# Performance work log

Measured on AMD Instinct MI355X. Metric: run time of the kernel, lower is better.

Reference implementation:

```python
import jax, jax.numpy as jnp
import numpy as np

N_LAYERS, D_MODEL, D_INNER, D_STATE, DT_RANK, D_CONV, VOCAB = 4, 768, 1536, 16, 48, 4, 32000
B, L = 2, 512
EPS = 1e-5


def rmsnorm(x, w):
    var = jnp.mean(jnp.square(x), axis=-1, keepdims=True)
    return x * jax.lax.rsqrt(var + EPS) * w


def mamba_mixer(x, in_w, cw, cb, xp_w, dtp_w, dtp_b, A_log, D_sk, out_w):
    # x: [B, L, D]
    proj = x @ in_w.T                                   # [B, L, 2*d_inner]
    h, gate = jnp.split(proj, 2, axis=-1)
    hc = jnp.transpose(h, (0, 2, 1))                    # [B, d_inner, L]
    hc = jax.lax.conv_general_dilated(
        hc, cw[:, None, :], (1,), [(D_CONV - 1, 0)],
        dimension_numbers=('NCH', 'OIH', 'NCH'),
        feature_group_count=D_INNER) + cb[None, :, None]  # causal depthwise conv
    h = jax.nn.silu(jnp.transpose(hc, (0, 2, 1)))       # [B, L, d_inner]
    ssm = h @ xp_w.T                                    # [B, L, dt_rank + 2*d_state]
    dt, Bm, Cm = jnp.split(ssm, [DT_RANK, DT_RANK + D_STATE], axis=-1)
    dt = jax.nn.softplus(dt @ dtp_w.T + dtp_b)          # [B, L, d_inner]
    A = -jnp.exp(A_log)                                 # [d_inner, d_state], always negative
    dA = jnp.exp(dt[..., None] * A)                     # [B, L, d_inner, d_state]
    dBu = (dt * h)[..., None] * Bm[:, :, None, :]       # [B, L, d_inner, d_state]

    def step(state, inp):
        dA_t, dBu_t, C_t = inp
        state = dA_t * state + dBu_t                    # [B, d_inner, d_state]
        return state, jnp.einsum('bds,bs->bd', state, C_t)

    xs = (jnp.moveaxis(dA, 1, 0), jnp.moveaxis(dBu, 1, 0), jnp.moveaxis(Cm, 1, 0))
    init = jnp.zeros((x.shape[0], D_INNER, D_STATE), dtype=x.dtype)
    _, ys = jax.lax.scan(step, init, xs)                # ys: [L, B, d_inner]
    y = jnp.moveaxis(ys, 0, 1) + D_sk * h
    y = y * jax.nn.silu(gate)
    return y @ out_w.T                                  # [B, L, D]


def setup_inputs() -> dict:
    key = jax.random.key(0)
    ks = jax.random.split(key, 8)
    inp = {
        'input_ids': jax.random.randint(ks[0], (B, L), 0, VOCAB, dtype=jnp.int32),
        'embed': jax.random.normal(ks[1], (VOCAB, D_MODEL), jnp.float32) * 0.02,
        'norm_f_w': jnp.ones((D_MODEL,), jnp.float32),
        'in_proj_w': jax.random.normal(ks[2], (N_LAYERS, 2 * D_INNER, D_MODEL), jnp.float32) * (D_MODEL ** -0.5),
        'conv_w': jax.random.normal(ks[3], (N_LAYERS, D_INNER, D_CONV), jnp.float32) * 0.3,
        'conv_b': jnp.zeros((N_LAYERS, D_INNER), jnp.float32),
        'x_proj_w': jax.random.normal(ks[4], (N_LAYERS, DT_RANK + 2 * D_STATE, D_INNER), jnp.float32) * (D_INNER ** -0.5),
        'dt_proj_w': jax.random.normal(ks[5], (N_LAYERS, D_INNER, DT_RANK), jnp.float32) * (DT_RANK ** -0.5),
        'dt_proj_b': jax.random.normal(ks[6], (N_LAYERS, D_INNER), jnp.float32) * 0.1,
        'A_log': jnp.broadcast_to(jnp.log(jnp.arange(1, D_STATE + 1, dtype=jnp.float32)), (N_LAYERS, D_INNER, D_STATE)).copy(),
        'D_skip': jnp.ones((N_LAYERS, D_INNER), jnp.float32),
        'out_proj_w': jax.random.normal(ks[7], (N_LAYERS, D_MODEL, D_INNER), jnp.float32) * (D_INNER ** -0.5),
        'norm_w': jnp.ones((N_LAYERS, D_MODEL), jnp.float32),
    }
    return inp


def reference(input_ids, embed, norm_f_w, in_proj_w, conv_w, conv_b,
              x_proj_w, dt_proj_w, dt_proj_b, A_log, D_skip, out_proj_w, norm_w):
    h = embed[input_ids]                                # [B, L, D]
    for i in range(N_LAYERS):
        h = h + mamba_mixer(rmsnorm(h, norm_w[i]), in_proj_w[i], conv_w[i], conv_b[i],
                            x_proj_w[i], dt_proj_w[i], dt_proj_b[i],
                            A_log[i], D_skip[i], out_proj_w[i])
    h = rmsnorm(h, norm_f_w)
    return h @ embed.T                                  # tied lm head logits [B, L, VOCAB]
```

## Files before the change

### kernel.cpp

```cpp
#include <hip/hip_runtime.h>
#include <hip/hip_bf16.h>
#include <math.h>

#define NL 4
#define DM 768
#define DI 1536
#define DS 16
#define DTR 48
#define DCONV 4
#define VOCAB_ 32000
#define BB 2
#define LL 512
#define ROWS (BB*LL)
#define SSMW (DTR + 2*DS)
#define NC 32
#define CL (LL/NC)
#define NDB (DI/16)
#define XP_KS 16
#define XP_KC (DI/XP_KS)
#define OP_KS 4
#define OP_KC (DI/OP_KS)

typedef __bf16 bf16x8 __attribute__((ext_vector_type(8)));
typedef float f32x4 __attribute__((ext_vector_type(4)));

__device__ __forceinline__ unsigned short f2bf(float f) {
    unsigned u = __float_as_uint(f);
    u = u + 0x7fffu + ((u >> 16) & 1u);
    return (unsigned short)(u >> 16);
}
__device__ __forceinline__ float bf2f(unsigned short b) {
    return __uint_as_float((unsigned)b << 16);
}

__global__ __launch_bounds__(256) void split_kernel(
    const float* __restrict__ x,
    unsigned short* __restrict__ hi, unsigned short* __restrict__ lo, int n4)
{
    int i = blockIdx.x * 256 + threadIdx.x;
    if (i >= n4) return;
    const float4 v = ((const float4*)x)[i];
    float vv[4] = {v.x, v.y, v.z, v.w};
    unsigned short hh[4], ll[4];
    #pragma unroll
    for (int j = 0; j < 4; j++) {
        hh[j] = f2bf(vv[j]);
        ll[j] = f2bf(vv[j] - bf2f(hh[j]));
    }
    ((ushort4*)hi)[i] = make_ushort4(hh[0], hh[1], hh[2], hh[3]);
    ((ushort4*)lo)[i] = make_ushort4(ll[0], ll[1], ll[2], ll[3]);
}

__device__ __forceinline__ void gld16(void* l, const void* g) {
    __builtin_amdgcn_global_load_lds(
        (const __attribute__((address_space(1))) void*)g,
        (__attribute__((address_space(3))) void*)l, 16, 0, 0);
}

template<int EPI>
__global__ __launch_bounds__(256) void gemm_mfma(
    const unsigned short* __restrict__ Ahi, const unsigned short* __restrict__ Alo, int lda,
    const unsigned short* __restrict__ Bhi, const unsigned short* __restrict__ Blo, int ldb,
    float* __restrict__ C, int ldc, int K,
    const float* __restrict__ resid, int gx, size_t zstride)
{
    __shared__ __align__(16) unsigned short sAh[128*32];
    __shared__ __align__(16) unsigned short sAl[128*32];
    __shared__ __align__(16) unsigned short sBh[128*32];
    __shared__ __align__(16) unsigned short sBl[128*32];

    const int tid  = threadIdx.x;
    const int lane = tid & 63;
    const int nb = gridDim.x;
    const int v  = (blockIdx.x & 7) * (nb >> 3) + (blockIdx.x >> 3);
    const int m0 = (v % gx) * 128;
    const int n0 = (v / gx) * 128;
    const int kb = (int)blockIdx.y * K;
    C += (size_t)blockIdx.y * zstride;

    const int w  = tid >> 6;
    const int wr = (w >> 1) * 64;
    const int wc = (w & 1) * 64;

    f32x4 acc[4][4];
    #pragma unroll
    for (int i = 0; i < 4; i++)
        #pragma unroll
        for (int j = 0; j < 4; j++)
            acc[i][j] = (f32x4){0.f, 0.f, 0.f, 0.f};

    const int srow = tid >> 2;
    const int ps   = tid & 3;
    const int lsl  = ps ^ ((srow >> 1) & 3);

    int offA[4], offB[4];
    #pragma unroll
    for (int i = 0; i < 4; i++) {
        int ra = wr + i*16 + (lane & 15);
        int pa = (lane >> 4) ^ ((ra >> 1) & 3);
        offA[i] = ra*32 + pa*8;
        int rb = wc + i*16 + (lane & 15);
        int pb = (lane >> 4) ^ ((rb >> 1) & 3);
        offB[i] = rb*32 + pb*8;
    }

    for (int k0 = kb; k0 < kb + K; k0 += 32) {
        const size_t a1 = (size_t)(m0 + srow)      * lda + k0 + lsl*8;
        const size_t a2 = (size_t)(m0 + 64 + srow) * lda + k0 + lsl*8;
        const size_t b1 = (size_t)(n0 + srow)      * ldb + k0 + lsl*8;
        const size_t b2 = (size_t)(n0 + 64 + srow) * ldb + k0 + lsl*8;
        gld16(&sAh[(size_t)tid*8],       Ahi + a1);
        gld16(&sAh[(size_t)(256+tid)*8], Ahi + a2);
        gld16(&sAl[(size_t)tid*8],       Alo + a1);
        gld16(&sAl[(size_t)(256+tid)*8], Alo + a2);
        gld16(&sBh[(size_t)tid*8],       Bhi + b1);
        gld16(&sBh[(size_t)(256+tid)*8], Bhi + b2);
        gld16(&sBl[(size_t)tid*8],       Blo + b1);
        gld16(&sBl[(size_t)(256+tid)*8], Blo + b2);
        __syncthreads();

        bf16x8 ah[4], al[4], bh[4], bl[4];
        #pragma unroll
        for (int i = 0; i < 4; i++) {
            ah[i] = *(const bf16x8*)&sAh[offA[i]];
            al[i] = *(const bf16x8*)&sAl[offA[i]];
            bh[i] = *(const bf16x8*)&sBh[offB[i]];
            bl[i] = *(const bf16x8*)&sBl[offB[i]];
        }
        #pragma unroll
        for (int i = 0; i < 4; i++)
            #pragma unroll
            for (int j = 0; j < 4; j++) {
                acc[i][j] = __builtin_amdgcn_mfma_f32_16x16x32_bf16(ah[i], bh[j], acc[i][j], 0, 0, 0);
                acc[i][j] = __builtin_amdgcn_mfma_f32_16x16x32_bf16(ah[i], bl[j], acc[i][j], 0, 0, 0);
                acc[i][j] = __builtin_amdgcn_mfma_f32_16x16x32_bf16(al[i], bh[j], acc[i][j], 0, 0, 0);
            }
        __syncthreads();
    }

    #pragma unroll
    for (int i = 0; i < 4; i++) {
        int rbase = m0 + wr + i*16 + (lane >> 4)*4;
        #pragma unroll
        for (int j = 0; j < 4; j++) {
            int col = n0 + wc + j*16 + (lane & 15);
            #pragma unroll
            for (int r = 0; r < 4; r++) {
                float vv = acc[i][j][r];
                if (EPI == 2) vv += resid[(size_t)(rbase + r)*ldc + col];
                C[(size_t)(rbase + r)*ldc + col] = vv;
            }
        }
    }
}

__global__ __launch_bounds__(256) void opart_reduce_kernel(
    const float* __restrict__ part, float* __restrict__ h, int n)
{
    int i = blockIdx.x * 256 + threadIdx.x;
    if (i >= n) return;
    float s = h[i];
    #pragma unroll
    for (int z = 0; z < OP_KS; ++z)
        s += part[(size_t)z * n + i];
    h[i] = s;
}

__global__ __launch_bounds__(256) void gather_kernel(
    const int* __restrict__ ids, const float* __restrict__ embed,
    float* __restrict__ h, int n)
{
    int idx = blockIdx.x * 256 + threadIdx.x;
    if (idx >= n) return;
    int d = idx % DM;
    int tok = idx / DM;
    h[idx] = embed[(size_t)ids[tok] * DM + d];
}

__global__ __launch_bounds__(256) void rmsnorm_kernel(
    const float* __restrict__ x, const float* __restrict__ w,
    float* __restrict__ out, int D)
{
    int row = blockIdx.x;
    const float* xr = x + (size_t)row * D;
    float ss = 0.f;
    for (int i = threadIdx.x; i < D; i += 256) { float v = xr[i]; ss += v * v; }
    for (int o = 32; o >= 1; o >>= 1) ss += __shfl_xor(ss, o, 64);
    __shared__ float sbuf[4];
    int wid = threadIdx.x >> 6;
    if ((threadIdx.x & 63) == 0) sbuf[wid] = ss;
    __syncthreads();
    if (threadIdx.x == 0) {
        float t = sbuf[0] + sbuf[1] + sbuf[2] + sbuf[3];
        sbuf[0] = 1.0f / sqrtf(t / (float)D + 1e-5f);
    }
    __syncthreads();
    float scale = sbuf[0];
    for (int i = threadIdx.x; i < D; i += 256)
        out[(size_t)row * D + i] = xr[i] * scale * w[i];
}

__global__ __launch_bounds__(256) void rmsnorm_split_kernel(
    const float* __restrict__ x, const float* __restrict__ w,
    unsigned short* __restrict__ hi, unsigned short* __restrict__ lo, int D)
{
    int row = blockIdx.x;
    const float* xr = x + (size_t)row * D;
    float ss = 0.f;
    for (int i = threadIdx.x; i < D; i += 256) { float v = xr[i]; ss += v * v; }
    for (int o = 32; o >= 1; o >>= 1) ss += __shfl_xor(ss, o, 64);
    __shared__ float sbuf[4];
    int wid = threadIdx.x >> 6;
    if ((threadIdx.x & 63) == 0) sbuf[wid] = ss;
    __syncthreads();
    if (threadIdx.x == 0) {
        float t = sbuf[0] + sbuf[1] + sbuf[2] + sbuf[3];
        sbuf[0] = 1.0f / sqrtf(t / (float)D + 1e-5f);
    }
    __syncthreads();
    float scale = sbuf[0];
    for (int i = threadIdx.x; i < D; i += 256) {
        float v = xr[i] * scale * w[i];
        unsigned short hh = f2bf(v);
        hi[(size_t)row * D + i] = hh;
        lo[(size_t)row * D + i] = f2bf(v - bf2f(hh));
    }
}

template<int EPI>
__global__ __launch_bounds__(256) void gemm_tn(
    const float* __restrict__ A, int lda,
    const float* __restrict__ W, int ldw,
    float* __restrict__ C, int ldc,
    int M, int N, int K,
    const float* __restrict__ bias,
    const float* __restrict__ resid)
{
    const int tid = threadIdx.x;
    const int tx = tid & 15;
    const int ty = tid >> 4;
    const int m0 = blockIdx.x * 64;
    const int n0 = blockIdx.y * 64;

    __shared__ float As[16][65];
    __shared__ float Ws[16][65];

    float acc[4][4];
    #pragma unroll
    for (int i = 0; i < 4; i++)
        #pragma unroll
        for (int j = 0; j < 4; j++) acc[i][j] = 0.f;

    const int lrow = tid >> 2;
    const int lk   = (tid & 3) * 4;

    for (int k0 = 0; k0 < K; k0 += 16) {
        {
            int m = m0 + lrow;
            int n = n0 + lrow;
            #pragma unroll
            for (int j = 0; j < 4; j++) {
                int k = k0 + lk + j;
                As[lk + j][lrow] = (m < M && k < K) ? A[(size_t)m * lda + k] : 0.f;
                Ws[lk + j][lrow] = (n < N && k < K) ? W[(size_t)n * ldw + k] : 0.f;
            }
        }
        __syncthreads();
        #pragma unroll
        for (int k = 0; k < 16; k++) {
            float a[4], wv[4];
            #pragma unroll
            for (int i = 0; i < 4; i++) a[i] = As[k][ty * 4 + i];
            #pragma unroll
            for (int j = 0; j < 4; j++) wv[j] = Ws[k][tx * 4 + j];
            #pragma unroll
            for (int i = 0; i < 4; i++)
                #pragma unroll
                for (int j = 0; j < 4; j++)
                    acc[i][j] += a[i] * wv[j];
        }
        __syncthreads();
    }

    #pragma unroll
    for (int i = 0; i < 4; i++) {
        int m = m0 + ty * 4 + i;
        if (m >= M) continue;
        #pragma unroll
        for (int j = 0; j < 4; j++) {
            int n = n0 + tx * 4 + j;
            if (n >= N) continue;
            float v = acc[i][j];
            if (EPI == 1) {
                v += bias[n];
                v = fmaxf(v, 0.f) + log1pf(expf(-fabsf(v)));
            }
            if (EPI == 2) v += resid[(size_t)m * ldc + n];
            C[(size_t)m * ldc + n] = v;
        }
    }
}

__global__ __launch_bounds__(256) void xproj_partial_kernel(
    const float* __restrict__ A,
    const float* __restrict__ W,
    float* __restrict__ part)
{
    __shared__ float sA[32*97];
    __shared__ float sW[80*97];
    const int m0 = blockIdx.x * 32;
    const int k0 = blockIdx.y * XP_KC;

    for (int idx = threadIdx.x; idx < 32*XP_KC; idx += 256) {
        int r = idx / XP_KC, k = idx % XP_KC;
        sA[r*97 + k] = A[(size_t)(m0 + r)*DI + k0 + k];
    }
    for (int idx = threadIdx.x; idx < 80*XP_KC; idx += 256) {
        int r = idx / XP_KC, k = idx % XP_KC;
        sW[r*97 + k] = W[(size_t)r*DI + k0 + k];
    }
    __syncthreads();

    const int tr = (threadIdx.x >> 4) * 2;
    const int tc = (threadIdx.x & 15) * 5;
    float acc[2][5];
    #pragma unroll
    for (int i = 0; i < 2; i++)
        #pragma unroll
        for (int j = 0; j < 5; j++) acc[i][j] = 0.f;

    #pragma unroll 4
    for (int k = 0; k < XP_KC; ++k) {
        float a0 = sA[tr*97 + k];
        float a1 = sA[(tr+1)*97 + k];
        float w0 = sW[(tc+0)*97 + k];
        float w1 = sW[(tc+1)*97 + k];
        float w2 = sW[(tc+2)*97 + k];
        float w3 = sW[(tc+3)*97 + k];
        float w4 = sW[(tc+4)*97 + k];
        acc[0][0] += a0*w0; acc[0][1] += a0*w1; acc[0][2] += a0*w2;
        acc[0][3] += a0*w3; acc[0][4] += a0*w4;
        acc[1][0] += a1*w0; acc[1][1] += a1*w1; acc[1][2] += a1*w2;
        acc[1][3] += a1*w3; acc[1][4] += a1*w4;
    }

    float* pp = part + ((size_t)blockIdx.y * ROWS + m0) * SSMW;
    #pragma unroll
    for (int i = 0; i < 2; i++)
        #pragma unroll
        for (int j = 0; j < 5; j++)
            pp[(size_t)(tr + i)*SSMW + tc + j] = acc[i][j];
}

__global__ __launch_bounds__(256) void xproj_reduce_kernel(
    const float* __restrict__ part, float* __restrict__ ssmout)
{
    int i = blockIdx.x * 256 + threadIdx.x;
    if (i >= ROWS * SSMW) return;
    float s = 0.f;
    #pragma unroll
    for (int ks = 0; ks < XP_KS; ++ks)
        s += part[(size_t)ks * ROWS * SSMW + i];
    ssmout[i] = s;
}

__global__ __launch_bounds__(256) void conv_silu_kernel(
    const float* __restrict__ proj,
    const float* __restrict__ cw, const float* __restrict__ cb,
    float* __restrict__ hconv)
{
    int idx = blockIdx.x * 256 + threadIdx.x;
    if (idx >= ROWS * DI) return;
    int d = idx % DI;
    int bt = idx / DI;
    int t = bt % LL;
    float sum = cb[d];
    #pragma unroll
    for (int j = 0; j < DCONV; j++) {
        int tt = t - (DCONV - 1) + j;
        if (tt >= 0)
            sum += cw[d * DCONV + j] * proj[(size_t)(bt - (DCONV - 1) + j) * (2 * DI) + d];
    }
    float sig = 1.f / (1.f + expf(-sum));
    hconv[idx] = sum * sig;
}

__global__ __launch_bounds__(256) void scan_local_kernel(
    const float* __restrict__ dt, const float* __restrict__ hconv,
    const float* __restrict__ ssm, const float* __restrict__ A_log,
    float* __restrict__ ylocal, float* __restrict__ E, float* __restrict__ P)
{
    const int tid = threadIdx.x;
    const int s  = tid & 15;
    const int dg = tid >> 4;
    int blk = blockIdx.x;
    const int dblk = blk % NDB; blk /= NDB;
    const int c = blk % NC;
    const int b = blk / NC;
    const int d = dblk * 16 + dg;

    const float Ads = -expf(A_log[(size_t)d * DS + s]);
    float state = 0.f, Ssum = 0.f;
    const int t0 = c * CL;
    const float* dtp = dt     + ((size_t)b*LL + t0)*DI + d;
    const float* hp  = hconv  + ((size_t)b*LL + t0)*DI + d;
    const float* sp  = ssm    + ((size_t)b*LL + t0)*SSMW;
    float*       yp  = ylocal + ((size_t)b*LL + t0)*DI + d;

    for (int t = 0; t < CL; ++t) {
        float dtv = dtp[(size_t)t * DI];
        float hv  = hp[(size_t)t * DI];
        float Bv  = sp[(size_t)t * SSMW + DTR + s];
        float Cv  = sp[(size_t)t * SSMW + DTR + DS + s];
        float dA  = expf(dtv * Ads);
        state = dA * state + dtv * hv * Bv;
        Ssum += dtv;
        float contrib = state * Cv;
        contrib += __shfl_xor(contrib, 1, 16);
        contrib += __shfl_xor(contrib, 2, 16);
        contrib += __shfl_xor(contrib, 4, 16);
        contrib += __shfl_xor(contrib, 8, 16);
        if (s == 0) yp[(size_t)t * DI] = contrib;
    }
    const size_t si = (((size_t)b*NC + c)*DI + d)*DS + s;
    E[si] = state;
    P[si] = expf(Ads * Ssum);
}

__global__ __launch_bounds__(256) void scan_carry_kernel(
    const float* __restrict__ E, const float* __restrict__ P,
    float* __restrict__ carry)
{
    int g = blockIdx.x * 256 + threadIdx.x;
    if (g >= BB * DI * DS) return;
    int b   = g / (DI * DS);
    int dsi = g % (DI * DS);
    float cv = 0.f;
    for (int c = 0; c < NC; ++c) {
        size_t idx = ((size_t)b*NC + c)*(DI*DS) + dsi;
        carry[idx] = cv;
        cv = P[idx] * cv + E[idx];
    }
}

template<int PLANES>
__global__ __launch_bounds__(256) void scan_fix_kernel(
    const float* __restrict__ dt, const float* __restrict__ hconv,
    const float* __restrict__ ssm, const float* __restrict__ proj,
    const float* __restrict__ A_log, const float* __restrict__ D_skip,
    const float* __restrict__ carry, float* __restrict__ y,
    unsigned short* __restrict__ yhi, unsigned short* __restrict__ ylo)
{
    const int tid = threadIdx.x;
    const int s  = tid & 15;
    const int dg = tid >> 4;
    int blk = blockIdx.x;
    const int dblk = blk % NDB; blk /= NDB;
    const int c = blk % NC;
    const int b = blk / NC;
    const int d = dblk * 16 + dg;

    const float Ads = -expf(A_log[(size_t)d * DS + s]);
    const float Dd  = D_skip[d];
    const float cv  = carry[(((size_t)b*NC + c)*DI + d)*DS + s];
    float S = 0.f;
    const int t0 = c * CL;
    const float* dtp = dt    + ((size_t)b*LL + t0)*DI + d;
    const float* hp  = hconv + ((size_t)b*LL + t0)*DI + d;
    const float* sp  = ssm   + ((size_t)b*LL + t0)*SSMW;
    const float* gp  = proj  + ((size_t)b*LL + t0)*(2*DI) + DI + d;
    const size_t yoff = ((size_t)b*LL + t0)*DI + d;

    for (int t = 0; t < CL; ++t) {
        float dtv = dtp[(size_t)t * DI];
        S += dtv;
        float Cv = sp[(size_t)t * SSMW + DTR + DS + s];
        float contrib = expf(Ads * S) * cv * Cv;
        contrib += __shfl_xor(contrib, 1, 16);
        contrib += __shfl_xor(contrib, 2, 16);
        contrib += __shfl_xor(contrib, 4, 16);
        contrib += __shfl_xor(contrib, 8, 16);
        if (s == 0) {
            float hv  = hp[(size_t)t * DI];
            float ylv = y[yoff + (size_t)t * DI];
            float gv  = gp[(size_t)t * (2*DI)];
            float sig = 1.f / (1.f + expf(-gv));
            float yv  = (ylv + contrib + Dd * hv) * (gv * sig);
            if (PLANES) {
                unsigned short hh = f2bf(yv);
                yhi[yoff + (size_t)t * DI] = hh;
                ylo[yoff + (size_t)t * DI] = f2bf(yv - bf2f(hh));
            } else {
                y[yoff + (size_t)t * DI] = yv;
            }
        }
    }
}

extern "C" void kernel_launch(void* const* d_in, const int* in_sizes, int n_in,
                              void* d_out, int out_size, void* d_ws, size_t ws_size,
                              hipStream_t stream)
{
    const int*   ids        = (const int*)  d_in[0];
    const float* embed      = (const float*)d_in[1];
    const float* norm_f_w   = (const float*)d_in[2];
    const float* in_proj_w  = (const float*)d_in[3];
    const float* conv_w     = (const float*)d_in[4];
    const float* conv_b     = (const float*)d_in[5];
    const float* x_proj_w   = (const float*)d_in[6];
    const float* dt_proj_w  = (const float*)d_in[7];
    const float* dt_proj_b  = (const float*)d_in[8];
    const float* A_log      = (const float*)d_in[9];
    const float* D_skip     = (const float*)d_in[10];
    const float* out_proj_w = (const float*)d_in[11];
    const float* norm_w     = (const float*)d_in[12];
    float* out = (float*)d_out;

    float* ws    = (float*)d_ws;
    float* h     = ws;
    float* xn    = h     + ROWS * DM;
    float* proj  = xn    + ROWS * DM;
    float* hconv = proj  + ROWS * 2 * DI;
    float* ssm   = hconv + ROWS * DI;
    float* dtb   = ssm   + ROWS * SSMW;
    float* yb    = dtb   + ROWS * DI;
    float* Ebuf  = yb    + ROWS * DI;
    float* Pbuf  = Ebuf  + (size_t)BB*NC*DI*DS;
    float* cbuf  = Pbuf  + (size_t)BB*NC*DI*DS;
    float* xpart = cbuf  + (size_t)BB*NC*DI*DS;
    float* opart = xpart + (size_t)XP_KS*ROWS*SSMW;
    const size_t F32_FLOATS = (size_t)ROWS * (DM + DM + 2*DI + DI + SSMW + DI + DI)
                            + 3 * (size_t)BB*NC*DI*DS
                            + (size_t)XP_KS*ROWS*SSMW
                            + (size_t)OP_KS*ROWS*DM;

    const size_t IPW_E = (size_t)NL * 2 * DI * DM;
    const size_t OPW_E = (size_t)NL * DM * DI;
    const size_t ACT_E = (size_t)ROWS * DI;
    const size_t EMB_E = (size_t)VOCAB_ * DM;
    unsigned short* u0   = (unsigned short*)(ws + F32_FLOATS);
    unsigned short* ipwh = u0;
    unsigned short* ipwl = ipwh + IPW_E;
    unsigned short* opwh = ipwl + IPW_E;
    unsigned short* opwl = opwh + OPW_E;
    unsigned short* acth = opwl + OPW_E;
    unsigned short* actl = acth + ACT_E;
    unsigned short* embh = actl + ACT_E;
    unsigned short* embl = embh + EMB_E;
    const size_t NEED_PROJ = F32_FLOATS*4 + 2*2*(IPW_E + OPW_E + ACT_E);
    const size_t NEED_HEAD = NEED_PROJ + 2*2*EMB_E;
    const bool mfma_proj = ws_size >= NEED_PROJ;
    const bool mfma_head = ws_size >= NEED_HEAD;

    gather_kernel<<<(ROWS * DM + 255) / 256, 256, 0, stream>>>(ids, embed, h, ROWS * DM);

    if (mfma_proj) {
        split_kernel<<<(int)(IPW_E/4 + 255)/256, 256, 0, stream>>>(in_proj_w,  ipwh, ipwl, (int)(IPW_E/4));
        split_kernel<<<(int)(OPW_E/4 + 255)/256, 256, 0, stream>>>(out_proj_w, opwh, opwl, (int)(OPW_E/4));
    }
    if (mfma_head) {
        split_kernel<<<(int)(EMB_E/4 + 255)/256, 256, 0, stream>>>(embed, embh, embl, (int)(EMB_E/4));
    }

    for (int i = 0; i < NL; ++i) {
        const float* ipw = in_proj_w  + (size_t)i * 2 * DI * DM;
        const float* cw  = conv_w     + (size_t)i * DI * DCONV;
        const float* cb  = conv_b     + (size_t)i * DI;
        const float* xpw = x_proj_w   + (size_t)i * SSMW * DI;
        const float* dpw = dt_proj_w  + (size_t)i * DI * DTR;
        const float* dpb = dt_proj_b  + (size_t)i * DI;
        const float* al  = A_log      + (size_t)i * DI * DS;
        const float* dsk = D_skip     + (size_t)i * DI;
        const float* opw = out_proj_w + (size_t)i * DM * DI;
        const float* nw  = norm_w     + (size_t)i * DM;

        if (mfma_proj) {
            rmsnorm_split_kernel<<<ROWS, 256, 0, stream>>>(h, nw, acth, actl, DM);
            gemm_mfma<0><<<dim3(8*24, 1), 256, 0, stream>>>(
                acth, actl, DM, ipwh + (size_t)i*2*DI*DM, ipwl + (size_t)i*2*DI*DM, DM,
                proj, 2*DI, DM, nullptr, 8, 0);
        } else {
            rmsnorm_kernel<<<ROWS, 256, 0, stream>>>(h, nw, xn, DM);
            gemm_tn<0><<<dim3(ROWS/64, (2*DI)/64), 256, 0, stream>>>(
                xn, DM, ipw, DM, proj, 2*DI, ROWS, 2*DI, DM, nullptr, nullptr);
        }

        conv_silu_kernel<<<(ROWS * DI + 255) / 256, 256, 0, stream>>>(proj, cw, cb, hconv);

        xproj_partial_kernel<<<dim3(ROWS/32, XP_KS), 256, 0, stream>>>(hconv, xpw, xpart);
        xproj_reduce_kernel<<<(ROWS*SSMW + 255)/256, 256, 0, stream>>>(xpart, ssm);

        gemm_tn<1><<<dim3(ROWS / 64, DI / 64), 256, 0, stream>>>(
            ssm, SSMW, dpw, DTR, dtb, DI, ROWS, DI, DTR, dpb, nullptr);

        scan_local_kernel<<<BB*NC*NDB, 256, 0, stream>>>(dtb, hconv, ssm, al, yb, Ebuf, Pbuf);
        scan_carry_kernel<<<(BB*DI*DS + 255)/256, 256, 0, stream>>>(Ebuf, Pbuf, cbuf);

        if (mfma_proj) {
            scan_fix_kernel<1><<<BB*NC*NDB, 256, 0, stream>>>(
                dtb, hconv, ssm, proj, al, dsk, cbuf, yb, acth, actl);
            gemm_mfma<0><<<dim3(8*6, OP_KS), 256, 0, stream>>>(
                acth, actl, DI, opwh + (size_t)i*DM*DI, opwl + (size_t)i*DM*DI, DI,
                opart, DM, OP_KC, nullptr, 8, (size_t)ROWS*DM);
            opart_reduce_kernel<<<(ROWS*DM + 255)/256, 256, 0, stream>>>(opart, h, ROWS*DM);
        } else {
            scan_fix_kernel<0><<<BB*NC*NDB, 256, 0, stream>>>(
                dtb, hconv, ssm, proj, al, dsk, cbuf, yb, nullptr, nullptr);
            gemm_tn<2><<<dim3(ROWS/64, DM/64), 256, 0, stream>>>(
                yb, DI, opw, DI, h, DM, ROWS, DM, DI, nullptr, h);
        }
    }

    if (mfma_head) {
        rmsnorm_split_kernel<<<ROWS, 256, 0, stream>>>(h, norm_f_w, acth, actl, DM);
        gemm_mfma<0><<<dim3(8*250, 1), 256, 0, stream>>>(
            acth, actl, DM, embh, embl, DM, out, VOCAB_, DM, nullptr, 8, 0);
    } else {
        rmsnorm_kernel<<<ROWS, 256, 0, stream>>>(h, norm_f_w, xn, DM);
        gemm_tn<0><<<dim3(ROWS/64, VOCAB_/64), 256, 0, stream>>>(
            xn, DM, embed, DM, out, VOCAB_, ROWS, VOCAB_, DM, nullptr, nullptr);
    }
}
```

Before: 1.238 ms.

## Fuse reductions with norms, dt projection, and fold scan carry into fix kernel

Merges the embedding gather with the first RMSNorm+bf16 split, and the out-projection partial reduction with the next layer's (or final) RMSNorm+split. Fuses the x_proj split-K reduction with the dt projection GEMM and softplus. Removes the separate scan carry kernel by having each scan_fix block recompute its chunk carry serially from E/P. This cuts kernel launches and intermediate round trips, at the cost of redundant carry recomputation and x_proj reductions across blocks. If the workspace is too small for the MFMA path but large enough for the MFMA head, the head may read an uninitialised normalised buffer.

Measured after the change: 1.226 ms. Within noise of the previous version (-1.0%).

```diff
diff --git a/kernel.cpp b/kernel.cpp
--- a/kernel.cpp
+++ b/kernel.cpp
@@ -20,6 +20,7 @@
 #define XP_KC (DI/XP_KS)
 #define OP_KS 4
 #define OP_KC (DI/OP_KS)
+#define DTB 96
 
 typedef __bf16 bf16x8 __attribute__((ext_vector_type(8)));
 typedef float f32x4 __attribute__((ext_vector_type(4)));
@@ -154,18 +155,6 @@
     }
 }
 
-__global__ __launch_bounds__(256) void opart_reduce_kernel(
-    const float* __restrict__ part, float* __restrict__ h, int n)
-{
-    int i = blockIdx.x * 256 + threadIdx.x;
-    if (i >= n) return;
-    float s = h[i];
-    #pragma unroll
-    for (int z = 0; z < OP_KS; ++z)
-        s += part[(size_t)z * n + i];
-    h[i] = s;
-}
-
 __global__ __launch_bounds__(256) void gather_kernel(
     const int* __restrict__ ids, const float* __restrict__ embed,
     float* __restrict__ h, int n)
@@ -175,6 +164,77 @@
     int d = idx % DM;
     int tok = idx / DM;
     h[idx] = embed[(size_t)ids[tok] * DM + d];
+}
+
+__global__ __launch_bounds__(256) void gather_norm_kernel(
+    const int* __restrict__ ids, const float* __restrict__ embed,
+    const float* __restrict__ w, float* __restrict__ h,
+    unsigned short* __restrict__ hi, unsigned short* __restrict__ lo)
+{
+    __shared__ float buf[DM];
+    __shared__ float sbuf[4];
+    const int row = blockIdx.x;
+    const int tok = ids[row];
+    float ss = 0.f;
+    for (int i = threadIdx.x; i < DM; i += 256) {
+        float v = embed[(size_t)tok*DM + i];
+        h[(size_t)row*DM + i] = v;
+        buf[i] = v;
+        ss += v*v;
+    }
+    for (int o = 32; o >= 1; o >>= 1) ss += __shfl_xor(ss, o, 64);
+    int wid = threadIdx.x >> 6;
+    if ((threadIdx.x & 63) == 0) sbuf[wid] = ss;
+    __syncthreads();
+    if (threadIdx.x == 0) {
+        float t = sbuf[0]+sbuf[1]+sbuf[2]+sbuf[3];
+        sbuf[0] = 1.0f / sqrtf(t/(float)DM + 1e-5f);
+    }
+    __syncthreads();
+    float scale = sbuf[0];
+    for (int i = threadIdx.x; i < DM; i += 256) {
+        float v = buf[i]*scale*w[i];
+        unsigned short hh = f2bf(v);
+        hi[(size_t)row*DM+i] = hh;
+        lo[(size_t)row*DM+i] = f2bf(v - bf2f(hh));
+    }
+}
+
+__global__ __launch_bounds__(256) void opreduce_norm_kernel(
+    const float* __restrict__ part,
+    const float* __restrict__ w,
+    float* __restrict__ h,
+    unsigned short* __restrict__ hi, unsigned short* __restrict__ lo)
+{
+    __shared__ float buf[DM];
+    __shared__ float sbuf[4];
+    const int row = blockIdx.x;
+    float ss = 0.f;
+    for (int i = threadIdx.x; i < DM; i += 256) {
+        float v = h[(size_t)row*DM + i];
+        #pragma unroll
+        for (int z = 0; z < OP_KS; ++z)
+            v += part[(size_t)z*ROWS*DM + (size_t)row*DM + i];
+        h[(size_t)row*DM + i] = v;
+        buf[i] = v;
+        ss += v*v;
+    }
+    for (int o = 32; o >= 1; o >>= 1) ss += __shfl_xor(ss, o, 64);
+    int wid = threadIdx.x >> 6;
+    if ((threadIdx.x & 63) == 0) sbuf[wid] = ss;
+    __syncthreads();
+    if (threadIdx.x == 0) {
+        float t = sbuf[0]+sbuf[1]+sbuf[2]+sbuf[3];
+        sbuf[0] = 1.0f / sqrtf(t/(float)DM + 1e-5f);
+    }
+    __syncthreads();
+    float scale = sbuf[0];
+    for (int i = threadIdx.x; i < DM; i += 256) {
+        float v = buf[i]*scale*w[i];
+        unsigned short hh = f2bf(v);
+        hi[(size_t)row*DM+i] = hh;
+        lo[(size_t)row*DM+i] = f2bf(v - bf2f(hh));
+    }
 }
 
 __global__ __launch_bounds__(256) void rmsnorm_kernel(
@@ -198,33 +258,6 @@
     float scale = sbuf[0];
     for (int i = threadIdx.x; i < D; i += 256)
         out[(size_t)row * D + i] = xr[i] * scale * w[i];
-}
-
-__global__ __launch_bounds__(256) void rmsnorm_split_kernel(
-    const float* __restrict__ x, const float* __restrict__ w,
-    unsigned short* __restrict__ hi, unsigned short* __restrict__ lo, int D)
-{
-    int row = blockIdx.x;
-    const float* xr = x + (size_t)row * D;
-    float ss = 0.f;
-    for (int i = threadIdx.x; i < D; i += 256) { float v = xr[i]; ss += v * v; }
-    for (int o = 32; o >= 1; o >>= 1) ss += __shfl_xor(ss, o, 64);
-    __shared__ float sbuf[4];
-    int wid = threadIdx.x >> 6;
-    if ((threadIdx.x & 63) == 0) sbuf[wid] = ss;
-    __syncthreads();
-    if (threadIdx.x == 0) {
-        float t = sbuf[0] + sbuf[1] + sbuf[2] + sbuf[3];
-        sbuf[0] = 1.0f / sqrtf(t / (float)D + 1e-5f);
-    }
-    __syncthreads();
-    float scale = sbuf[0];
-    for (int i = threadIdx.x; i < D; i += 256) {
-        float v = xr[i] * scale * w[i];
-        unsigned short hh = f2bf(v);
-        hi[(size_t)row * D + i] = hh;
-        lo[(size_t)row * D + i] = f2bf(v - bf2f(hh));
-    }
 }
 
 template<int EPI>
@@ -352,16 +385,71 @@
             pp[(size_t)(tr + i)*SSMW + tc + j] = acc[i][j];
 }
 
-__global__ __launch_bounds__(256) void xproj_reduce_kernel(
-    const float* __restrict__ part, float* __restrict__ ssmout)
-{
-    int i = blockIdx.x * 256 + threadIdx.x;
-    if (i >= ROWS * SSMW) return;
-    float s = 0.f;
-    #pragma unroll
-    for (int ks = 0; ks < XP_KS; ++ks)
-        s += part[(size_t)ks * ROWS * SSMW + i];
-    ssmout[i] = s;
+__global__ __launch_bounds__(256) void xred_dtproj_kernel(
+    const float* __restrict__ part,
+    const float* __restrict__ dpw,
+    const float* __restrict__ dpb,
+    float* __restrict__ ssmout,
+    float* __restrict__ dtb)
+{
+    __shared__ float sA[32*81];
+    __shared__ float sW[DTB*49];
+    const int m0 = blockIdx.x * 32;
+    const int n0 = blockIdx.y * DTB;
+
+    if (blockIdx.y == 0) {
+        for (int idx = threadIdx.x; idx < 32*SSMW; idx += 256) {
+            int r = idx / SSMW, cc = idx % SSMW;
+            float s = 0.f;
+            #pragma unroll
+            for (int ks = 0; ks < XP_KS; ++ks)
+                s += part[(size_t)ks*ROWS*SSMW + (size_t)(m0+r)*SSMW + cc];
+            if (cc < DTR) sA[r*81 + cc] = s;
+            ssmout[(size_t)(m0+r)*SSMW + cc] = s;
+        }
+    } else {
+        for (int idx = threadIdx.x; idx < 32*DTR; idx += 256) {
+            int r = idx / DTR, cc = idx % DTR;
+            float s = 0.f;
+            #pragma unroll
+            for (int ks = 0; ks < XP_KS; ++ks)
+                s += part[(size_t)ks*ROWS*SSMW + (size_t)(m0+r)*SSMW + cc];
+            sA[r*81 + cc] = s;
+        }
+    }
+    for (int idx = threadIdx.x; idx < DTB*DTR; idx += 256) {
+        int n = idx / DTR, k = idx % DTR;
+        sW[n*49 + k] = dpw[(size_t)(n0+n)*DTR + k];
+    }
+    __syncthreads();
+
+    const int tr = (threadIdx.x >> 4) * 2;
+    const int tc = (threadIdx.x & 15) * 6;
+    float acc[2][6];
+    #pragma unroll
+    for (int i = 0; i < 2; i++)
+        #pragma unroll
+        for (int j = 0; j < 6; j++) acc[i][j] = 0.f;
+
+    #pragma unroll 4
+    for (int k = 0; k < DTR; ++k) {
+        float a0 = sA[tr*81 + k];
+        float a1 = sA[(tr+1)*81 + k];
+        #pragma unroll
+        for (int j = 0; j < 6; ++j) {
+            float wv = sW[(tc+j)*49 + k];
+            acc[0][j] += a0*wv;
+            acc[1][j] += a1*wv;
+        }
+    }
+    #pragma unroll
+    for (int i = 0; i < 2; ++i)
+        #pragma unroll
+        for (int j = 0; j < 6; ++j) {
+            float v = acc[i][j] + dpb[n0 + tc + j];
+            v = fmaxf(v, 0.f) + log1pf(expf(-fabsf(v)));
+            dtb[(size_t)(m0 + tr + i)*DI + n0 + tc + j] = v;
+        }
 }
 
 __global__ __launch_bounds__(256) void conv_silu_kernel(
@@ -427,28 +515,13 @@
     P[si] = expf(Ads * Ssum);
 }
 
-__global__ __launch_bounds__(256) void scan_carry_kernel(
-    const float* __restrict__ E, const float* __restrict__ P,
-    float* __restrict__ carry)
-{
-    int g = blockIdx.x * 256 + threadIdx.x;
-    if (g >= BB * DI * DS) return;
-    int b   = g / (DI * DS);
-    int dsi = g % (DI * DS);
-    float cv = 0.f;
-    for (int c = 0; c < NC; ++c) {
-        size_t idx = ((size_t)b*NC + c)*(DI*DS) + dsi;
-        carry[idx] = cv;
-        cv = P[idx] * cv + E[idx];
-    }
-}
-
 template<int PLANES>
 __global__ __launch_bounds__(256) void scan_fix_kernel(
     const float* __restrict__ dt, const float* __restrict__ hconv,
     const float* __restrict__ ssm, const float* __restrict__ proj,
     const float* __restrict__ A_log, const float* __restrict__ D_skip,
-    const float* __restrict__ carry, float* __restrict__ y,
+    const float* __restrict__ E, const float* __restrict__ P,
+    float* __restrict__ y,
     unsigned short* __restrict__ yhi, unsigned short* __restrict__ ylo)
 {
     const int tid = threadIdx.x;
@@ -462,7 +535,16 @@
 
     const float Ads = -expf(A_log[(size_t)d * DS + s]);
     const float Dd  = D_skip[d];
-    const float cv  = carry[(((size_t)b*NC + c)*DI + d)*DS + s];
+
+    float cv = 0.f;
+    {
+        const size_t epbase = ((size_t)b*NC)*(size_t)(DI*DS) + (size_t)d*DS + s;
+        for (int j = 0; j < c; ++j) {
+            size_t idx = epbase + (size_t)j*(DI*DS);
+            cv = P[idx] * cv + E[idx];
+        }
+    }
+
     float S = 0.f;
     const int t0 = c * CL;
     const float* dtp = dt    + ((size_t)b*LL + t0)*DI + d;
@@ -526,11 +608,10 @@
     float* yb    = dtb   + ROWS * DI;
     float* Ebuf  = yb    + ROWS * DI;
     float* Pbuf  = Ebuf  + (size_t)BB*NC*DI*DS;
-    float* cbuf  = Pbuf  + (size_t)BB*NC*DI*DS;
-    float* xpart = cbuf  + (size_t)BB*NC*DI*DS;
+    float* xpart = Pbuf  + (size_t)BB*NC*DI*DS;
     float* opart = xpart + (size_t)XP_KS*ROWS*SSMW;
     const size_t F32_FLOATS = (size_t)ROWS * (DM + DM + 2*DI + DI + SSMW + DI + DI)
-                            + 3 * (size_t)BB*NC*DI*DS
+                            + 2 * (size_t)BB*NC*DI*DS
                             + (size_t)XP_KS*ROWS*SSMW
                             + (size_t)OP_KS*ROWS*DM;
 
@@ -552,11 +633,12 @@
     const bool mfma_proj = ws_size >= NEED_PROJ;
     const bool mfma_head = ws_size >= NEED_HEAD;
 
-    gather_kernel<<<(ROWS * DM + 255) / 256, 256, 0, stream>>>(ids, embed, h, ROWS * DM);
-
     if (mfma_proj) {
         split_kernel<<<(int)(IPW_E/4 + 255)/256, 256, 0, stream>>>(in_proj_w,  ipwh, ipwl, (int)(IPW_E/4));
         split_kernel<<<(int)(OPW_E/4 + 255)/256, 256, 0, stream>>>(out_proj_w, opwh, opwl, (int)(OPW_E/4));
+        gather_norm_kernel<<<ROWS, 256, 0, stream>>>(ids, embed, norm_w, h, acth, actl);
+    } else {
+        gather_kernel<<<(ROWS * DM + 255) / 256, 256, 0, stream>>>(ids, embed, h, ROWS * DM);
     }
     if (mfma_head) {
         split_kernel<<<(int)(EMB_E/4 + 255)/256, 256, 0, stream>>>(embed, embh, embl, (int)(EMB_E/4));
@@ -572,15 +654,14 @@
         const float* al  = A_log      + (size_t)i * DI * DS;
         const float* dsk = D_skip     + (size_t)i * DI;
         const float* opw = out_proj_w + (size_t)i * DM * DI;
-        const float* nw  = norm_w     + (size_t)i * DM;
+        const float* nwNext = (i < NL-1) ? (norm_w + (size_t)(i+1) * DM) : norm_f_w;
 
         if (mfma_proj) {
-            rmsnorm_split_kernel<<<ROWS, 256, 0, stream>>>(h, nw, acth, actl, DM);
             gemm_mfma<0><<<dim3(8*24, 1), 256, 0, stream>>>(
                 acth, actl, DM, ipwh + (size_t)i*2*DI*DM, ipwl + (size_t)i*2*DI*DM, DM,
                 proj, 2*DI, DM, nullptr, 8, 0);
         } else {
-            rmsnorm_kernel<<<ROWS, 256, 0, stream>>>(h, nw, xn, DM);
+            rmsnorm_kernel<<<ROWS, 256, 0, stream>>>(h, norm_w + (size_t)i*DM, xn, DM);
             gemm_tn<0><<<dim3(ROWS/64, (2*DI)/64), 256, 0, stream>>>(
                 xn, DM, ipw, DM, proj, 2*DI, ROWS, 2*DI, DM, nullptr, nullptr);
         }
@@ -588,31 +669,26 @@
         conv_silu_kernel<<<(ROWS * DI + 255) / 256, 256, 0, stream>>>(proj, cw, cb, hconv);
 
         xproj_partial_kernel<<<dim3(ROWS/32, XP_KS), 256, 0, stream>>>(hconv, xpw, xpart);
-        xproj_reduce_kernel<<<(ROWS*SSMW + 255)/256, 256, 0, stream>>>(xpart, ssm);
-
-        gemm_tn<1><<<dim3(ROWS / 64, DI / 64), 256, 0, stream>>>(
-            ssm, SSMW, dpw, DTR, dtb, DI, ROWS, DI, DTR, dpb, nullptr);
+        xred_dtproj_kernel<<<dim3(ROWS/32, DI/DTB), 256, 0, stream>>>(xpart, dpw, dpb, ssm, dtb);
 
         scan_local_kernel<<<BB*NC*NDB, 256, 0, stream>>>(dtb, hconv, ssm, al, yb, Ebuf, Pbuf);
-        scan_carry_kernel<<<(BB*DI*DS + 255)/256, 256, 0, stream>>>(Ebuf, Pbuf, cbuf);
 
         if (mfma_proj) {
             scan_fix_kernel<1><<<BB*NC*NDB, 256, 0, stream>>>(
-                dtb, hconv, ssm, proj, al, dsk, cbuf, yb, acth, actl);
+                dtb, hconv, ssm, proj, al, dsk, Ebuf, Pbuf, yb, acth, actl);
             gemm_mfma<0><<<dim3(8*6, OP_KS), 256, 0, stream>>>(
                 acth, actl, DI, opwh + (size_t)i*DM*DI, opwl + (size_t)i*DM*DI, DI,
                 opart, DM, OP_KC, nullptr, 8, (size_t)ROWS*DM);
-            opart_reduce_kernel<<<(ROWS*DM + 255)/256, 256, 0, stream>>>(opart, h, ROWS*DM);
+            opreduce_norm_kernel<<<ROWS, 256, 0, stream>>>(opart, nwNext, h, acth, actl);
         } else {
             scan_fix_kernel<0><<<BB*NC*NDB, 256, 0, stream>>>(
-                dtb, hconv, ssm, proj, al, dsk, cbuf, yb, nullptr, nullptr);
+                dtb, hconv, ssm, proj, al, dsk, Ebuf, Pbuf, yb, nullptr, nullptr);
             gemm_tn<2><<<dim3(ROWS/64, DM/64), 256, 0, stream>>>(
                 yb, DI, opw, DI, h, DM, ROWS, DM, DI, nullptr, h);
         }
     }
 
     if (mfma_head) {
-        rmsnorm_split_kernel<<<ROWS, 256, 0, stream>>>(h, norm_f_w, acth, actl, DM);
         gemm_mfma<0><<<dim3(8*250, 1), 256, 0, stream>>>(
             acth, actl, DM, embh, embl, DM, out, VOCAB_, DM, nullptr, 8, 0);
     } else {
```
